# Kernel tuning notes

Measured on AMD Instinct MI355X. Metric: run time of the kernel, lower is better.

The kernel has to match this reference:

```python
import jax, jax.numpy as jnp
import numpy as np

T, B, A, OBS = 128, 16, 32, 256
K, NACT, HID = 3, 9, 32


def setup_inputs() -> dict:
    key = jax.random.key(0)
    ks = jax.random.split(key, 12)
    sc = 0.1  # small init scale for stability
    d = {}
    d["x"] = jax.random.normal(ks[0], (T, B, A, OBS), jnp.float32)
    d["done"] = jax.random.randint(ks[1], (T, B), 0, 2, jnp.int32)
    d["actions"] = jax.random.randint(ks[2], (T, B, A, K), 0, NACT, jnp.int32)
    d["W1"] = sc * jax.random.normal(ks[3], (128, OBS), jnp.float32)
    d["b1"] = jnp.zeros((128,), jnp.float32)
    d["W2"] = sc * jax.random.normal(ks[4], (128, 128), jnp.float32)
    d["b2"] = jnp.zeros((128,), jnp.float32)
    d["W3"] = sc * jax.random.normal(ks[5], (64, 128), jnp.float32)
    d["b3"] = jnp.zeros((64,), jnp.float32)
    d["Wih"] = sc * jax.random.normal(ks[6], (4 * HID, 64), jnp.float32)
    d["Whh"] = sc * jax.random.normal(ks[7], (4 * HID, HID), jnp.float32)
    d["bih"] = jnp.zeros((4 * HID,), jnp.float32)
    d["bhh"] = jnp.zeros((4 * HID,), jnp.float32)
    d["Wh"] = sc * jax.random.normal(ks[8], (K, NACT, HID), jnp.float32)
    d["bh"] = jnp.zeros((K, NACT), jnp.float32)
    d["h0"] = jnp.zeros((B * A, HID), jnp.float32)
    d["c0"] = jnp.zeros((B * A, HID), jnp.float32)
    return d


def _forward(x, done, actions, W1, b1, W2, b2, W3, b3,
             Wih, Whh, bih, bhh, Wh, bh, h0, c0):
    # MLP trunk: n_obs -> 128 -> 128 -> 64 (tanh, tanh, linear)
    z = jnp.tanh(x @ W1.T + b1)
    z = jnp.tanh(z @ W2.T + b2)
    z = z @ W3.T + b3                       # [T, B, A, 64]
    zf = z.reshape(T, B * A, 64)
    # done[t] repeated per agent (repeat_interleave along batch*agent axis)
    done_f = jnp.repeat(done.astype(x.dtype), A, axis=1)  # [T, B*A]

    def step(carry, inp):
        h, c = carry
        zt, dt = inp                        # [B*A,64], [B*A]
        mask = (1.0 - dt)[:, None]
        h = h * mask
        c = c * mask
        gates = zt @ Wih.T + bih + h @ Whh.T + bhh  # [B*A, 4H]
        i, f, g, o = jnp.split(gates, 4, axis=-1)   # PyTorch gate order i,f,g,o
        i, f, o = jax.nn.sigmoid(i), jax.nn.sigmoid(f), jax.nn.sigmoid(o)
        g = jnp.tanh(g)
        c = f * c + i * g
        h = o * jnp.tanh(c)
        return (h, c), h

    (_, _), ys = jax.lax.scan(step, (h0, c0), (zf, done_f))
    y = ys.reshape(T, B, A, HID)
    # multi-head categorical logits: stacked heads [K, NACT, HID]
    logits = jnp.einsum('tbah,knh->tbakn', y, Wh) + bh  # [T,B,A,K,NACT]
    lp = jax.nn.log_softmax(logits, axis=-1)
    entropies = -jnp.sum(jnp.exp(lp) * lp, axis=-1)     # [T,B,A,K]
    alp = jnp.take_along_axis(lp, actions[..., None], axis=-1)[..., 0]  # [T,B,A,K]
    logprobs = jnp.prod(alp, axis=-1)  # faithful: product of per-head log-probs
    return logprobs, entropies


def reference(x, done, actions, W1, b1, W2, b2, W3, b3,
              Wih, Whh, bih, bhh, Wh, bh, h0, c0):
    logprobs, entropies = _forward(x, done, actions, W1, b1, W2, b2, W3, b3,
                                   Wih, Whh, bih, bhh, Wh, bh, h0, c0)
    return actions, logprobs, entropies
```

## Files before the change

kernel.cpp:

```cpp
#include <hip/hip_runtime.h>
#include <math.h>

namespace {
constexpr int Tn = 128, Bn = 16, An = 32, OBS = 256, Kh = 3, NACT = 9, HID = 32;
constexpr int TBA = Tn * Bn * An;
constexpr int BA  = Bn * An;
constexpr int OUT_LP  = TBA * Kh;
constexpr int OUT_ENT = TBA * Kh + TBA;
constexpr int NCHUNK = 32;
constexpr int CHUNKW = Tn / NCHUNK;

constexpr int W1_OFF  = 0;
constexpr int W2_OFF  = 32768;
constexpr int W3_OFF  = 49152;
constexpr int WIH_OFF = 57344;
constexpr int W16_TOT = 65536;

typedef __fp16   pk16x2 __attribute__((ext_vector_type(2)));
typedef _Float16 half8v __attribute__((ext_vector_type(8)));
typedef float    f32x4  __attribute__((ext_vector_type(4)));
}

__device__ __forceinline__ float fast_sig(float x) {
  return __builtin_amdgcn_rcpf(1.f + __expf(-x));
}
__device__ __forceinline__ float fast_tanh(float x) {
  return fmaf(2.f, fast_sig(2.f * x), -1.f);
}
__device__ __forceinline__ unsigned h2bits(pk16x2 h) {
  return __builtin_bit_cast(unsigned, h);
}
__device__ __forceinline__ pk16x2 bits2h(unsigned u) {
  return __builtin_bit_cast(pk16x2, u);
}
__device__ __forceinline__ int first_done_ge(unsigned long long dm0,
                                             unsigned long long dm1, int n) {
  unsigned long long m0 = (n < 64) ? (dm0 & (~0ull << n)) : 0ull;
  unsigned long long m1 = (n < 64) ? dm1 : (dm1 & (~0ull << (n - 64)));
  if (m0) return __builtin_ctzll(m0);
  if (m1) return 64 + __builtin_ctzll(m1);
  return 128;
}

__global__ __launch_bounds__(256) void cvtw_act_kernel(
    const float* __restrict__ W1, const float* __restrict__ W2,
    const float* __restrict__ W3, const float* __restrict__ Wih,
    _Float16* __restrict__ w16, const float* __restrict__ Whh,
    const int* __restrict__ done, _Float16* __restrict__ wt16,
    unsigned long long* __restrict__ dmask)
{
  const int bid = blockIdx.x;
  const int tid = threadIdx.x;
  if (bid < W16_TOT/256) {
    int i = bid * 256 + tid;
    float v;
    if (i < W2_OFF)       v = W1[i];
    else if (i < W3_OFF)  v = W2[i - W2_OFF];
    else if (i < WIH_OFF) v = W3[i - W3_OFF];
    else                  v = Wih[i - WIH_OFF];
    w16[i] = (_Float16)v;
  } else {
    for (int i = tid; i < 4096; i += 256) {
      int tl = i >> 9, rem = i & 511, l = rem >> 3, j = rem & 7;
      int gate = 16*tl + (l & 15);
      int unit = ((l >> 4) << 3) + j;
      wt16[i] = (_Float16)Whh[gate*HID + unit];
    }
    if (tid < 64) {
#pragma unroll
      for (int b = 0; b < Bn; ++b) {
        unsigned long long m0 = __ballot(done[tid*Bn + b] != 0);
        unsigned long long m1 = __ballot(done[(tid + 64)*Bn + b] != 0);
        if (tid == 0) { dmask[2*b] = m0; dmask[2*b + 1] = m1; }
      }
    }
  }
}

template<int ROWS, int WSTR>
__device__ __forceinline__ void stage_wh(const _Float16* __restrict__ Wg, int kofs,
                                         _Float16* __restrict__ wt, int tid)
{
#pragma unroll
  for (int it = 0; it < ROWS/64; ++it) {
    int idx = tid + it*512;
    int o = idx >> 3, g8 = idx & 7;
    *(half8v*)&wt[o*72 + g8*8] =
        *(const half8v*)&Wg[(size_t)o*WSTR + kofs + g8*8];
  }
}

template<int NOC, int XSTR>
__device__ __forceinline__ void mfma_slab(const _Float16* __restrict__ xsrc,
                                          const _Float16* __restrict__ wt,
                                          int rA, int ln, int quad, f32x4 acc[8])
{
#pragma unroll
  for (int kc = 0; kc < 2; ++kc) {
    half8v a = *(const half8v*)&xsrc[rA*XSTR + kc*32 + quad*8];
#pragma unroll
    for (int oc = 0; oc < NOC; ++oc) {
      half8v b = *(const half8v*)&wt[(oc*16 + ln)*72 + kc*32 + quad*8];
      acc[oc] = __builtin_amdgcn_mfma_f32_16x16x32_f16(a, b, acc[oc], 0, 0, 0);
    }
  }
}

__global__ __launch_bounds__(512) void mlp_kernel(
    const float* __restrict__ x, const _Float16* __restrict__ w16,
    const float* __restrict__ b1, const float* __restrict__ b2,
    const float* __restrict__ b3, const float* __restrict__ bih,
    const float* __restrict__ bhh, uint2* __restrict__ G1q)
{
  __shared__ __align__(16) _Float16 xs[128*72];
  __shared__ __align__(16) _Float16 wt[128*72];
  __shared__ __align__(16) _Float16 act[128*136];
  const _Float16* W1h  = w16 + W1_OFF;
  const _Float16* W2h  = w16 + W2_OFF;
  const _Float16* W3h  = w16 + W3_OFF;
  const _Float16* Wihh = w16 + WIH_OFF;
  const int tid  = threadIdx.x;
  const int w    = tid >> 6;
  const int lane = tid & 63;
  const int ln   = lane & 15;
  const int quad = lane >> 4;
  const int rA   = 16*w + ln;
  const int r0   = 16*w + quad*4;
  const int R0   = blockIdx.x * 128;
  f32x4 acc[8];

#pragma unroll
  for (int oc = 0; oc < 8; ++oc) acc[oc] = (f32x4)0.f;
  for (int kt = 0; kt < 4; ++kt) {
#pragma unroll
    for (int it = 0; it < 2; ++it) {
      int idx = tid + it*512;
      int r = idx >> 3, g8 = idx & 7;
      const float* xp = &x[(size_t)(R0 + r)*OBS + kt*64 + g8*8];
      float4 v0 = *(const float4*)xp;
      float4 v1 = *(const float4*)(xp + 4);
      half8v hv = { (_Float16)v0.x, (_Float16)v0.y, (_Float16)v0.z, (_Float16)v0.w,
                    (_Float16)v1.x, (_Float16)v1.y, (_Float16)v1.z, (_Float16)v1.w };
      *(half8v*)&xs[r*72 + g8*8] = hv;
    }
    stage_wh<128, 256>(W1h, kt*64, wt, tid);
    __syncthreads();
    mfma_slab<8, 72>(xs, wt, rA, ln, quad, acc);
    __syncthreads();
  }
#pragma unroll
  for (int oc = 0; oc < 8; ++oc) {
    int o = oc*16 + ln;
    float bv = b1[o];
#pragma unroll
    for (int r = 0; r < 4; ++r)
      act[(r0 + r)*136 + o] = (_Float16)fast_tanh(acc[oc][r] + bv);
  }

#pragma unroll
  for (int oc = 0; oc < 8; ++oc) acc[oc] = (f32x4)0.f;
  for (int kt = 0; kt < 2; ++kt) {
    stage_wh<128, 128>(W2h, kt*64, wt, tid);
    __syncthreads();
    mfma_slab<8, 136>(act + kt*64, wt, rA, ln, quad, acc);
    __syncthreads();
  }
#pragma unroll
  for (int oc = 0; oc < 8; ++oc) {
    int o = oc*16 + ln;
    float bv = b2[o];
#pragma unroll
    for (int r = 0; r < 4; ++r)
      act[(r0 + r)*136 + o] = (_Float16)fast_tanh(acc[oc][r] + bv);
  }

#pragma unroll
  for (int oc = 0; oc < 4; ++oc) acc[oc] = (f32x4)0.f;
  for (int kt = 0; kt < 2; ++kt) {
    stage_wh<64, 128>(W3h, kt*64, wt, tid);
    __syncthreads();
    mfma_slab<4, 136>(act + kt*64, wt, rA, ln, quad, acc);
    __syncthreads();
  }
#pragma unroll
  for (int oc = 0; oc < 4; ++oc) {
    int o = oc*16 + ln;
    float bv = b3[o];
#pragma unroll
    for (int r = 0; r < 4; ++r)
      xs[(r0 + r)*72 + o] = (_Float16)(acc[oc][r] + bv);
  }

#pragma unroll
  for (int oc = 0; oc < 8; ++oc) acc[oc] = (f32x4)0.f;
  stage_wh<128, 64>(Wihh, 0, wt, tid);
  __syncthreads();
  mfma_slab<8, 72>(xs, wt, rA, ln, quad, acc);
#pragma unroll
  for (int p = 0; p < 2; ++p) {
    int ui = p*16 + ln;
    float bi = bih[ui]      + bhh[ui];
    float bf = bih[ui + 32] + bhh[ui + 32];
    float bg = bih[ui + 64] + bhh[ui + 64];
    float bo = bih[ui + 96] + bhh[ui + 96];
#pragma unroll
    for (int r = 0; r < 4; ++r) {
      int n = R0 + r0 + r;
      uint2 q;
      q.x = h2bits(__builtin_amdgcn_cvt_pkrtz(acc[p  ][r] + bi, acc[p+4][r] + bg));
      q.y = h2bits(__builtin_amdgcn_cvt_pkrtz(acc[p+2][r] + bf, acc[p+6][r] + bo));
      G1q[(size_t)n*32 + ui] = q;
    }
  }
}

__global__ __launch_bounds__(64) void lstm_kernel(
    const uint2* __restrict__ G1q, const _Float16* __restrict__ wt16,
    const unsigned long long* __restrict__ dmask,
    const float* __restrict__ h0, const float* __restrict__ c0,
    unsigned* __restrict__ Y16)
{
  static_assert(BA == 512 && NCHUNK == 32, "index math below assumes 512x32");
  const int lane = threadIdx.x;
  const int ln   = lane & 15;
  const int q    = lane >> 4;
  const int rg   = blockIdx.x & 31;
  const int ck   = blockIdx.x >> 5;
  const int R0   = rg * 16;
  const int b    = R0 >> 5;

  const unsigned long long dm0 = dmask[2*b];
  const unsigned long long dm1 = dmask[2*b + 1];

  const int s = (ck == 0) ? 0 : first_done_ge(dm0, dm1, ck * CHUNKW);
  const int e = (ck == NCHUNK - 1) ? Tn
                                   : first_done_ge(dm0, dm1, (ck + 1) * CHUNKW);
  if (s >= e) return;

  half8v wA0 = *(const half8v*)&wt16[0*512 + lane*8];
  half8v wA1 = *(const half8v*)&wt16[1*512 + lane*8];
  half8v wA2 = *(const half8v*)&wt16[2*512 + lane*8];
  half8v wA3 = *(const half8v*)&wt16[3*512 + lane*8];
  half8v wA4 = *(const half8v*)&wt16[4*512 + lane*8];
  half8v wA5 = *(const half8v*)&wt16[5*512 + lane*8];
  half8v wA6 = *(const half8v*)&wt16[6*512 + lane*8];
  half8v wA7 = *(const half8v*)&wt16[7*512 + lane*8];

  const float4 z4 = {0.f, 0.f, 0.f, 0.f};
  float4 cs0, cs1;
  unsigned w0, w1, w2, w3;
  if (ck == 0) {
    const float* hp = &h0[(size_t)(R0 + ln)*HID + 4*q];
    const float* cp = &c0[(size_t)(R0 + ln)*HID + 4*q];
    float4 ha = *(const float4*)hp;
    float4 hb = *(const float4*)(hp + 16);
    cs0 = *(const float4*)cp;
    cs1 = *(const float4*)(cp + 16);
    w0 = h2bits(__builtin_amdgcn_cvt_pkrtz(ha.x, ha.y));
    w1 = h2bits(__builtin_amdgcn_cvt_pkrtz(ha.z, ha.w));
    w2 = h2bits(__builtin_amdgcn_cvt_pkrtz(hb.x, hb.y));
    w3 = h2bits(__builtin_amdgcn_cvt_pkrtz(hb.z, hb.w));
  } else {
    cs0 = z4; cs1 = z4;
    w0 = w1 = w2 = w3 = 0u;
  }

  const int aA = (ln + ((q & 1) << 5)) << 2;
  const int aB = aA + (16 << 2);
  const bool loq = (q < 2);

  const uint2* gb = G1q + ((size_t)(R0 + ln) * 32 + 4*q);
  const size_t gstep = (size_t)BA * 32;

#define LOADG(T, A0, A1, A2, A3)                                  \
  { const uint2* p_ = gb + (size_t)(T) * gstep;                   \
    A0 = *(const uint4*)(p_);      A1 = *(const uint4*)(p_ + 2);  \
    A2 = *(const uint4*)(p_ + 16); A3 = *(const uint4*)(p_ + 18); }

  uint4 rc0, rc1, rc2, rc3;
  LOADG(s, rc0, rc1, rc2, rc3);

  for (int t = s; t < e; ++t) {
    int tn = (t + 1 < e) ? t + 1 : e - 1;
    uint4 rn0, rn1, rn2, rn3;
    LOADG(tn, rn0, rn1, rn2, rn3);

    unsigned long long dbit = (t < 64) ? (dm0 >> t) : (dm1 >> (t - 64));
    unsigned b0, b1, b2, b3;
    if (dbit & 1ull) {
      b0 = b1 = b2 = b3 = 0u;
      cs0 = z4; cs1 = z4;
    } else {
      unsigned e0 = (unsigned)__builtin_amdgcn_ds_bpermute(aA, (int)w0);
      unsigned e1 = (unsigned)__builtin_amdgcn_ds_bpermute(aA, (int)w1);
      unsigned e2 = (unsigned)__builtin_amdgcn_ds_bpermute(aA, (int)w2);
      unsigned e3 = (unsigned)__builtin_amdgcn_ds_bpermute(aA, (int)w3);
      unsigned o0 = (unsigned)__builtin_amdgcn_ds_bpermute(aB, (int)w0);
      unsigned o1 = (unsigned)__builtin_amdgcn_ds_bpermute(aB, (int)w1);
      unsigned o2 = (unsigned)__builtin_amdgcn_ds_bpermute(aB, (int)w2);
      unsigned o3 = (unsigned)__builtin_amdgcn_ds_bpermute(aB, (int)w3);
      b0 = loq ? e0 : e2;  b1 = loq ? e1 : e3;
      b2 = loq ? o0 : o2;  b3 = loq ? o1 : o3;
    }
    uint4 bu; bu.x = b0; bu.y = b1; bu.z = b2; bu.w = b3;
    half8v B = __builtin_bit_cast(half8v, bu);

    f32x4 ci0, cf0, cg0, co0, ci1, cf1, cg1, co1;
    {
      pk16x2 ig, fo;
      ig = bits2h(rc0.x); fo = bits2h(rc0.y);
      ci0[0] = ig.x; cg0[0] = ig.y; cf0[0] = fo.x; co0[0] = fo.y;
      ig = bits2h(rc0.z); fo = bits2h(rc0.w);
      ci0[1] = ig.x; cg0[1] = ig.y; cf0[1] = fo.x; co0[1] = fo.y;
      ig = bits2h(rc1.x); fo = bits2h(rc1.y);
      ci0[2] = ig.x; cg0[2] = ig.y; cf0[2] = fo.x; co0[2] = fo.y;
      ig = bits2h(rc1.z); fo = bits2h(rc1.w);
      ci0[3] = ig.x; cg0[3] = ig.y; cf0[3] = fo.x; co0[3] = fo.y;
      ig = bits2h(rc2.x); fo = bits2h(rc2.y);
      ci1[0] = ig.x; cg1[0] = ig.y; cf1[0] = fo.x; co1[0] = fo.y;
      ig = bits2h(rc2.z); fo = bits2h(rc2.w);
      ci1[1] = ig.x; cg1[1] = ig.y; cf1[1] = fo.x; co1[1] = fo.y;
      ig = bits2h(rc3.x); fo = bits2h(rc3.y);
      ci1[2] = ig.x; cg1[2] = ig.y; cf1[2] = fo.x; co1[2] = fo.y;
      ig = bits2h(rc3.z); fo = bits2h(rc3.w);
      ci1[3] = ig.x; cg1[3] = ig.y; cf1[3] = fo.x; co1[3] = fo.y;
    }

    f32x4 ai0 = __builtin_amdgcn_mfma_f32_16x16x32_f16(wA0, B, ci0, 0, 0, 0);
    f32x4 ai1 = __builtin_amdgcn_mfma_f32_16x16x32_f16(wA1, B, ci1, 0, 0, 0);
    f32x4 af0 = __builtin_amdgcn_mfma_f32_16x16x32_f16(wA2, B, cf0, 0, 0, 0);
    f32x4 af1 = __builtin_amdgcn_mfma_f32_16x16x32_f16(wA3, B, cf1, 0, 0, 0);
    f32x4 ag0 = __builtin_amdgcn_mfma_f32_16x16x32_f16(wA4, B, cg0, 0, 0, 0);
    f32x4 ag1 = __builtin_amdgcn_mfma_f32_16x16x32_f16(wA5, B, cg1, 0, 0, 0);
    f32x4 ao0 = __builtin_amdgcn_mfma_f32_16x16x32_f16(wA6, B, co0, 0, 0, 0);
    f32x4 ao1 = __builtin_amdgcn_mfma_f32_16x16x32_f16(wA7, B, co1, 0, 0, 0);

    f32x4 hva, hvb;
#pragma unroll
    for (int r = 0; r < 4; ++r) {
      float iv = fast_sig(ai0[r]);
      float fv = fast_sig(af0[r]);
      float gv = fast_tanh(ag0[r]);
      float ov = fast_sig(ao0[r]);
      float cc = fmaf(fv, cs0[r], iv * gv);
      cs0[r] = cc;
      hva[r] = ov * fast_tanh(cc);
    }
#pragma unroll
    for (int r = 0; r < 4; ++r) {
      float iv = fast_sig(ai1[r]);
      float fv = fast_sig(af1[r]);
      float gv = fast_tanh(ag1[r]);
      float ov = fast_sig(ao1[r]);
      float cc = fmaf(fv, cs1[r], iv * gv);
      cs1[r] = cc;
      hvb[r] = ov * fast_tanh(cc);
    }

    w0 = h2bits(__builtin_amdgcn_cvt_pkrtz(hva[0], hva[1]));
    w1 = h2bits(__builtin_amdgcn_cvt_pkrtz(hva[2], hva[3]));
    w2 = h2bits(__builtin_amdgcn_cvt_pkrtz(hvb[0], hvb[1]));
    w3 = h2bits(__builtin_amdgcn_cvt_pkrtz(hvb[2], hvb[3]));
    unsigned* yb = &Y16[((size_t)t*BA + R0 + ln)*16 + 2*q];
    uint2 ya; ya.x = w0; ya.y = w1;
    uint2 yc; yc.x = w2; yc.y = w3;
    *(uint2*)yb       = ya;
    *(uint2*)(yb + 8) = yc;

    rc0 = rn0; rc1 = rn1; rc2 = rn2; rc3 = rn3;
  }
#undef LOADG
}

__global__ __launch_bounds__(256) void head_kernel(
    const unsigned* __restrict__ Y16, const float* __restrict__ Wh,
    const float* __restrict__ bh, const int* __restrict__ actions,
    float* __restrict__ out)
{
  __shared__ __align__(16) float whs[27*32];
  __shared__ float bhs[32];
  const int tid = threadIdx.x;
  const int R0 = blockIdx.x * 256;
  for (int i = tid; i < 27*32; i += 256) whs[i] = Wh[i];
  if (tid < 27) bhs[tid] = bh[tid];
  const int row = R0 + tid;
  float yv[32];
#pragma unroll
  for (int i4 = 0; i4 < 4; ++i4) {
    uint4 yw = *(const uint4*)&Y16[(size_t)row*16 + i4*4];
    pk16x2 p0 = bits2h(yw.x), p1 = bits2h(yw.y), p2 = bits2h(yw.z), p3 = bits2h(yw.w);
    yv[i4*8+0] = (float)p0.x; yv[i4*8+1] = (float)p0.y;
    yv[i4*8+2] = (float)p1.x; yv[i4*8+3] = (float)p1.y;
    yv[i4*8+4] = (float)p2.x; yv[i4*8+5] = (float)p2.y;
    yv[i4*8+6] = (float)p3.x; yv[i4*8+7] = (float)p3.y;
  }
  __syncthreads();
  float l[27];
#pragma unroll
  for (int m = 0; m < 27; ++m) {
    float a = bhs[m];
#pragma unroll
    for (int k4 = 0; k4 < 8; ++k4) {
      float4 w4 = *(const float4*)&whs[m*32 + k4*4];
      a = fmaf(yv[k4*4+0], w4.x, a);
      a = fmaf(yv[k4*4+1], w4.y, a);
      a = fmaf(yv[k4*4+2], w4.z, a);
      a = fmaf(yv[k4*4+3], w4.w, a);
    }
    l[m] = a;
  }
  float logprob = 1.0f;
#pragma unroll
  for (int kk = 0; kk < 3; ++kk) {
    float mx = l[kk*9];
#pragma unroll
    for (int n = 1; n < 9; ++n) mx = fmaxf(mx, l[kk*9+n]);
    float s = 0.f;
#pragma unroll
    for (int n = 0; n < 9; ++n) s += __expf(l[kk*9+n] - mx);
    float lse = mx + __logf(s);
    float ent = 0.f;
#pragma unroll
    for (int n = 0; n < 9; ++n) {
      float lp = l[kk*9+n] - lse;
      ent -= __expf(lp) * lp;
    }
    int a = actions[row*3 + kk];
    out[row*3 + kk] = (float)a;
    float alp = 0.f;
#pragma unroll
    for (int n = 0; n < 9; ++n) alp = (a == n) ? (l[kk*9+n] - lse) : alp;
    logprob *= alp;
    out[OUT_ENT + row*3 + kk] = ent;
  }
  out[OUT_LP + row] = logprob;
}

extern "C" void kernel_launch(void* const* d_in, const int* in_sizes, int n_in,
                              void* d_out, int out_size, void* d_ws, size_t ws_size,
                              hipStream_t stream)
{
  const float* x       = (const float*)d_in[0];
  const int*   done    = (const int*)  d_in[1];
  const int*   actions = (const int*)  d_in[2];
  const float* W1  = (const float*)d_in[3];
  const float* b1  = (const float*)d_in[4];
  const float* W2  = (const float*)d_in[5];
  const float* b2  = (const float*)d_in[6];
  const float* W3  = (const float*)d_in[7];
  const float* b3  = (const float*)d_in[8];
  const float* Wih = (const float*)d_in[9];
  const float* Whh = (const float*)d_in[10];
  const float* bih = (const float*)d_in[11];
  const float* bhh = (const float*)d_in[12];
  const float* Wh  = (const float*)d_in[13];
  const float* bh  = (const float*)d_in[14];
  const float* h0  = (const float*)d_in[15];
  const float* c0  = (const float*)d_in[16];
  float* out = (float*)d_out;

  uint2* G1q = (uint2*)d_ws;
  unsigned* Y16 = (unsigned*)(G1q + (size_t)TBA*32);
  _Float16* W16 = (_Float16*)(Y16 + (size_t)TBA*16);
  _Float16* WT16 = W16 + W16_TOT;
  unsigned long long* Dm = (unsigned long long*)(WT16 + 4096);

  cvtw_act_kernel<<<W16_TOT/256 + 1, 256, 0, stream>>>(
      W1, W2, W3, Wih, W16, Whh, done, WT16, Dm);
  mlp_kernel<<<TBA/128, 512, 0, stream>>>(x, W16, b1, b2, b3, bih, bhh, G1q);
  lstm_kernel<<<32 * NCHUNK, 64, 0, stream>>>(G1q, WT16, Dm, h0, c0, Y16);
  head_kernel<<<TBA/256, 256, 0, stream>>>(Y16, Wh, bh, actions, out);
}
```

Measured before the change: 168.0 us.

## Double-buffer MLP weight staging and feed x directly into MFMA registers

The MLP kernel now uses two shared-memory weight buffers. It stages the next weight slab, including slabs from the following layer, while MFMAs run on the current one, which removes one barrier per k-step. The input rows of x are loaded straight into registers as the MFMA A operand, with the next tile prefetched a step ahead, so the LDS round trip for x goes away. A launch-bounds occupancy hint of 4 is also added. The cost is higher register pressure from the prefetched float4 values, which that occupancy hint may constrain.

```diff
diff --git a/kernel.cpp b/kernel.cpp
--- a/kernel.cpp
+++ b/kernel.cpp
@@ -106,14 +106,31 @@
   }
 }
 
-__global__ __launch_bounds__(512) void mlp_kernel(
+template<int NOC>
+__device__ __forceinline__ void mfma_regA(half8v a0, half8v a1,
+                                          const _Float16* __restrict__ wt,
+                                          int ln, int quad, f32x4 acc[8])
+{
+#pragma unroll
+  for (int oc = 0; oc < NOC; ++oc) {
+    half8v b = *(const half8v*)&wt[(oc*16 + ln)*72 + quad*8];
+    acc[oc] = __builtin_amdgcn_mfma_f32_16x16x32_f16(a0, b, acc[oc], 0, 0, 0);
+  }
+#pragma unroll
+  for (int oc = 0; oc < NOC; ++oc) {
+    half8v b = *(const half8v*)&wt[(oc*16 + ln)*72 + 32 + quad*8];
+    acc[oc] = __builtin_amdgcn_mfma_f32_16x16x32_f16(a1, b, acc[oc], 0, 0, 0);
+  }
+}
+
+__global__ __launch_bounds__(512, 4) void mlp_kernel(
     const float* __restrict__ x, const _Float16* __restrict__ w16,
     const float* __restrict__ b1, const float* __restrict__ b2,
     const float* __restrict__ b3, const float* __restrict__ bih,
     const float* __restrict__ bhh, uint2* __restrict__ G1q)
 {
-  __shared__ __align__(16) _Float16 xs[128*72];
-  __shared__ __align__(16) _Float16 wt[128*72];
+  __shared__ __align__(16) _Float16 wt0[128*72];
+  __shared__ __align__(16) _Float16 wt1[128*72];
   __shared__ __align__(16) _Float16 act[128*136];
   const _Float16* W1h  = w16 + W1_OFF;
   const _Float16* W2h  = w16 + W2_OFF;
@@ -128,26 +145,50 @@
   const int r0   = 16*w + quad*4;
   const int R0   = blockIdx.x * 128;
   f32x4 acc[8];
-
+  const float* xrow = &x[(size_t)(R0 + rA)*OBS + quad*8];
+
+#define XLOAD(KT, U0, U1, U2, U3) {                                   \
+    const float* xp_ = xrow + (KT)*64;                                \
+    U0 = *(const float4*)(xp_);      U1 = *(const float4*)(xp_ + 4);  \
+    U2 = *(const float4*)(xp_ + 32); U3 = *(const float4*)(xp_ + 36); }
+#define XCVT(U0, U1, U2, U3, A0, A1) {                                         \
+    A0 = (half8v){(_Float16)U0.x,(_Float16)U0.y,(_Float16)U0.z,(_Float16)U0.w, \
+                  (_Float16)U1.x,(_Float16)U1.y,(_Float16)U1.z,(_Float16)U1.w};\
+    A1 = (half8v){(_Float16)U2.x,(_Float16)U2.y,(_Float16)U2.z,(_Float16)U2.w, \
+                  (_Float16)U3.x,(_Float16)U3.y,(_Float16)U3.z,(_Float16)U3.w}; }
+
+  float4 u0, u1, u2, u3, v0, v1, v2, v3;
+  half8v a0, a1;
+
+  XLOAD(0, u0, u1, u2, u3);
+  stage_wh<128, 256>(W1h, 0, wt0, tid);
 #pragma unroll
   for (int oc = 0; oc < 8; ++oc) acc[oc] = (f32x4)0.f;
-  for (int kt = 0; kt < 4; ++kt) {
-#pragma unroll
-    for (int it = 0; it < 2; ++it) {
-      int idx = tid + it*512;
-      int r = idx >> 3, g8 = idx & 7;
-      const float* xp = &x[(size_t)(R0 + r)*OBS + kt*64 + g8*8];
-      float4 v0 = *(const float4*)xp;
-      float4 v1 = *(const float4*)(xp + 4);
-      half8v hv = { (_Float16)v0.x, (_Float16)v0.y, (_Float16)v0.z, (_Float16)v0.w,
-                    (_Float16)v1.x, (_Float16)v1.y, (_Float16)v1.z, (_Float16)v1.w };
-      *(half8v*)&xs[r*72 + g8*8] = hv;
-    }
-    stage_wh<128, 256>(W1h, kt*64, wt, tid);
-    __syncthreads();
-    mfma_slab<8, 72>(xs, wt, rA, ln, quad, acc);
-    __syncthreads();
-  }
+  __syncthreads();
+
+  stage_wh<128, 256>(W1h, 64, wt1, tid);
+  XLOAD(1, v0, v1, v2, v3);
+  XCVT(u0, u1, u2, u3, a0, a1);
+  mfma_regA<8>(a0, a1, wt0, ln, quad, acc);
+  __syncthreads();
+
+  stage_wh<128, 256>(W1h, 128, wt0, tid);
+  XLOAD(2, u0, u1, u2, u3);
+  XCVT(v0, v1, v2, v3, a0, a1);
+  mfma_regA<8>(a0, a1, wt1, ln, quad, acc);
+  __syncthreads();
+
+  stage_wh<128, 256>(W1h, 192, wt1, tid);
+  XLOAD(3, v0, v1, v2, v3);
+  XCVT(u0, u1, u2, u3, a0, a1);
+  mfma_regA<8>(a0, a1, wt0, ln, quad, acc);
+  __syncthreads();
+
+  stage_wh<128, 128>(W2h, 0, wt0, tid);
+  XCVT(v0, v1, v2, v3, a0, a1);
+  mfma_regA<8>(a0, a1, wt1, ln, quad, acc);
+  __syncthreads();
+
 #pragma unroll
   for (int oc = 0; oc < 8; ++oc) {
     int o = oc*16 + ln;
@@ -159,12 +200,14 @@
 
 #pragma unroll
   for (int oc = 0; oc < 8; ++oc) acc[oc] = (f32x4)0.f;
-  for (int kt = 0; kt < 2; ++kt) {
-    stage_wh<128, 128>(W2h, kt*64, wt, tid);
-    __syncthreads();
-    mfma_slab<8, 136>(act + kt*64, wt, rA, ln, quad, acc);
-    __syncthreads();
-  }
+  stage_wh<128, 128>(W2h, 64, wt1, tid);
+  mfma_slab<8, 136>(act, wt0, rA, ln, quad, acc);
+  __syncthreads();
+
+  stage_wh<64, 128>(W3h, 0, wt0, tid);
+  mfma_slab<8, 136>(act + 64, wt1, rA, ln, quad, acc);
+  __syncthreads();
+
 #pragma unroll
   for (int oc = 0; oc < 8; ++oc) {
     int o = oc*16 + ln;
@@ -176,26 +219,26 @@
 
 #pragma unroll
   for (int oc = 0; oc < 4; ++oc) acc[oc] = (f32x4)0.f;
-  for (int kt = 0; kt < 2; ++kt) {
-    stage_wh<64, 128>(W3h, kt*64, wt, tid);
-    __syncthreads();
-    mfma_slab<4, 136>(act + kt*64, wt, rA, ln, quad, acc);
-    __syncthreads();
-  }
+  stage_wh<64, 128>(W3h, 64, wt1, tid);
+  mfma_slab<4, 136>(act, wt0, rA, ln, quad, acc);
+  __syncthreads();
+
+  stage_wh<128, 64>(Wihh, 0, wt0, tid);
+  mfma_slab<4, 136>(act + 64, wt1, rA, ln, quad, acc);
+  __syncthreads();
+
 #pragma unroll
   for (int oc = 0; oc < 4; ++oc) {
     int o = oc*16 + ln;
     float bv = b3[o];
 #pragma unroll
     for (int r = 0; r < 4; ++r)
-      xs[(r0 + r)*72 + o] = (_Float16)(acc[oc][r] + bv);
+      act[(r0 + r)*136 + o] = (_Float16)(acc[oc][r] + bv);
   }
 
 #pragma unroll
   for (int oc = 0; oc < 8; ++oc) acc[oc] = (f32x4)0.f;
-  stage_wh<128, 64>(Wihh, 0, wt, tid);
-  __syncthreads();
-  mfma_slab<8, 72>(xs, wt, rA, ln, quad, acc);
+  mfma_slab<8, 136>(act, wt0, rA, ln, quad, acc);
 #pragma unroll
   for (int p = 0; p < 2; ++p) {
     int ui = p*16 + ln;
@@ -212,6 +255,8 @@
       G1q[(size_t)n*32 + ui] = q;
     }
   }
+#undef XLOAD
+#undef XCVT
 }
 
 __global__ __launch_bounds__(64) void lstm_kernel(
```

Result: no change. 168.6 us (+0.4%).
